# Kernel optimization log

Measured on AMD Instinct MI355X. Metric: run time of the kernel, lower is better.

Reference implementation:

```python
import jax, jax.numpy as jnp
import numpy as np

N = 1_048_576   # sampled points
E = 32          # grid feature dim (static_grid.out_dim / xyzt_grid.out_dim)
H = 64          # hidden_dim
GEO = 15        # geo_feat_dim
V = 3           # input_ch_views


def setup_inputs() -> dict:
    key = jax.random.key(0)
    ks = jax.random.split(key, 32)
    rn = lambda k, s: jax.random.normal(k, s, jnp.float32)
    w = lambda k, i, o: rn(k, (i, o)) * (1.0 / np.sqrt(i))
    inp = {
        'embedded_xyz': rn(ks[0], (N, E)),
        'embedded_xyzt': rn(ks[1], (N, E)),
        'embedded_xyzt_cam': rn(ks[2], (N, E)),
        'input_views': rn(ks[3], (N, V)),
        'keep_mask_bg': (jax.random.uniform(ks[4], (N,)) < 0.95).astype(jnp.float32),
        'keep_mask_fg': (jax.random.uniform(ks[5], (N,)) < 0.95).astype(jnp.float32),
        'keep_mask_actor': (jax.random.uniform(ks[6], (N,)) < 0.95).astype(jnp.float32),
    }
    # sigma nets: E->H, H->H, H->(1+1+GEO); color nets: in->H, H->H, H->H, H->3
    sigma_shapes = [(E, H), (H, H), (H, 1 + 1 + GEO)]
    bg_color_shapes = [(V + GEO, H), (H, H), (H, H), (H, 3)]      # BG uses viewdirs
    dyn_color_shapes = [(GEO, H), (H, H), (H, H), (H, 3)]          # use_viewdirs_FG=False
    ki = 7
    for pref, cshapes in (('bg', bg_color_shapes), ('fg', dyn_color_shapes), ('actor', dyn_color_shapes)):
        for l, (i, o) in enumerate(sigma_shapes):
            inp[f'{pref}_s{l}'] = w(ks[ki], i, o); ki += 1
        for l, (i, o) in enumerate(cshapes):
            inp[f'{pref}_c{l}'] = w(ks[ki], i, o); ki += 1
    return inp


def _mlp(h, Ws):
    # bias-free Linear + ReLU chain, no ReLU after last layer
    for W in Ws[:-1]:
        h = jax.nn.relu(h @ W)
    return h @ Ws[-1]


def _branch(emb, views, sW, cW, mask):
    h = _mlp(emb, sW)                       # [N, 1+1+GEO]
    sigma = jax.nn.softplus(h[:, 0]) * mask # relu_act = Softplus
    geo = h[:, 2:]
    ci = geo if views is None else jnp.concatenate([views, geo], axis=-1)
    color = jax.nn.sigmoid(_mlp(ci, cW)) * mask[:, None]
    return sigma, color


def reference(embedded_xyz, embedded_xyzt, embedded_xyzt_cam, input_views,
              keep_mask_bg, keep_mask_fg, keep_mask_actor,
              bg_s0, bg_s1, bg_s2, bg_c0, bg_c1, bg_c2, bg_c3,
              fg_s0, fg_s1, fg_s2, fg_c0, fg_c1, fg_c2, fg_c3,
              actor_s0, actor_s1, actor_s2, actor_c0, actor_c1, actor_c2, actor_c3):
    bg_sigma, bg_color = _branch(embedded_xyz, input_views,
                                 [bg_s0, bg_s1, bg_s2], [bg_c0, bg_c1, bg_c2, bg_c3], keep_mask_bg)
    fg_sigma, fg_color = _branch(embedded_xyzt, None,
                                 [fg_s0, fg_s1, fg_s2], [fg_c0, fg_c1, fg_c2, fg_c3], keep_mask_fg)
    ac_sigma, ac_color = _branch(embedded_xyzt_cam, None,
                                 [actor_s0, actor_s1, actor_s2], [actor_c0, actor_c1, actor_c2, actor_c3], keep_mask_actor)
    sigma = bg_sigma + fg_sigma + ac_sigma + 1e-9
    color = ((bg_sigma / sigma)[:, None] * bg_color
             + (fg_sigma / sigma)[:, None] * fg_color
             + (ac_sigma / sigma)[:, None] * ac_color)
    return jnp.concatenate([color, sigma[:, None]], axis=-1)  # [N, 4]
```

## Files before the change

### kernel.cpp

```cpp
#include <hip/hip_runtime.h>

typedef unsigned int  uint;
typedef unsigned short ushort;

#define N_PTS  1048576
#define BLOCK  1024
#define WAVES  16
#define NPT    2
#define CHUNK  (WAVES * NPT * 16)
#define NCHUNK (N_PTS / CHUNK)
#define GRID   256

static_assert(N_PTS % CHUNK == 0, "chunking");
static_assert(NCHUNK % GRID == 0, "grid stride");

typedef __attribute__((ext_vector_type(8))) _Float16 f16x8;
typedef __attribute__((ext_vector_type(2))) _Float16 f16x2;
typedef __attribute__((ext_vector_type(4))) float    f32x4;

struct Params {
    const float* emb[3];
    const float* views;
    const float* mask[3];
    const float* w[21];
    float* out;
};

__device__ uint g_wbuf[3 * 9216];

#define OFF_S0 0
#define OFF_S1 2048
#define OFF_S2 6144
#define OFF_C0 7168
#define OFF_C1 9216
#define OFF_C2 13312
#define OFF_C3 17408
#define BR_SZ  18432

__device__ __forceinline__ uint cvt2w(float a, float b) {
    f16x2 v = {(_Float16)a, (_Float16)b};
    return __builtin_bit_cast(uint, v);
}
__device__ __forceinline__ uint cvt2(float a, float b) {
    return __builtin_bit_cast(uint, __builtin_amdgcn_cvt_pkrtz(a, b));
}
__device__ __forceinline__ uint maxz(uint x) {
    f16x2 v = __builtin_bit_cast(f16x2, x);
    f16x2 z = {(_Float16)0.f, (_Float16)0.f};
    return __builtin_bit_cast(uint, __builtin_elementwise_max(v, z));
}

__device__ __forceinline__ f32x4 MFMA(f16x8 a, f16x8 b, f32x4 c) {
    return __builtin_amdgcn_mfma_f32_16x16x32_f16(a, b, c, 0, 0, 0);
}

__device__ __forceinline__ float fast_rcp(float x) { return __builtin_amdgcn_rcpf(x); }

__device__ __forceinline__ float wphys(int L, int br, const float* W, int kp, int m) {
    if (L == 0) return W[kp * 64 + m];
    const int g = (kp & 31) >> 3, e = kp & 7, h = kp >> 5;
    if (L == 3) {
        if (e < 4) {
            const int f = 4 * g + e;
            if (f < 1) return 0.f;
            return (br == 0) ? W[(f + 2) * 64 + m] : W[(f - 1) * 64 + m];
        }
        return (br == 0 && g == 0 && e <= 6) ? W[(e - 4) * 64 + m] : 0.f;
    }
    const int f = 16 * ((e >> 2) + 2 * h) + 4 * g + (e & 3);
    if (L == 2) return W[f * 17 + (m == 0 ? 0 : m + 1)];
    if (L == 6) return (m < 3) ? W[f * 3 + m] : 0.f;
    return W[f * 64 + m];
}

__global__ void prep_weights(Params P) {
    const int idx = blockIdx.x * 256 + threadIdx.x;
    const int br  = idx / 9216;
    const int rem = idx - br * 9216;
    int L, q;
    if      (rem < 1024) { L = 0; q = rem;        }
    else if (rem < 3072) { L = 1; q = rem - 1024; }
    else if (rem < 3584) { L = 2; q = rem - 3072; }
    else if (rem < 4608) { L = 3; q = rem - 3584; }
    else if (rem < 6656) { L = 4; q = rem - 4608; }
    else if (rem < 8704) { L = 5; q = rem - 6656; }
    else                 { L = 6; q = rem - 8704; }
    const float* W   = P.w[br * 7 + L];
    const int kk_n   = (L == 0 || L == 3) ? 1 : 2;
    const int E  = q * 2;
    const int b  = E >> 9;
    const int ln = (E >> 3) & 63;
    const int e  = E & 7;
    const int mt = b / kk_n;
    const int kk = b - mt * kk_n;
    const int m  = mt * 16 + (ln & 15);
    const int kp = kk * 32 + (ln >> 4) * 8 + e;
    g_wbuf[idx] = cvt2w(wphys(L, br, W, kp, m), wphys(L, br, W, kp + 1, m));
}

template<bool RELU>
__device__ __forceinline__ void handoff64(const f32x4 (&a)[4], uint4 &b0, uint4 &b1) {
#pragma unroll
    for (int h = 0; h < 2; ++h) {
        const f32x4 &lo = a[2 * h], &hi = a[2 * h + 1];
        uint w0 = cvt2(lo[0], lo[1]);
        uint w1 = cvt2(lo[2], lo[3]);
        uint w2 = cvt2(hi[0], hi[1]);
        uint w3 = cvt2(hi[2], hi[3]);
        if (RELU) { w0 = maxz(w0); w1 = maxz(w1); w2 = maxz(w2); w3 = maxz(w3); }
        uint4 &b = h ? b1 : b0;
        b.x = w0; b.y = w1; b.z = w2; b.w = w3;
    }
}

__device__ __forceinline__ void layer64(const ushort* lw, int lane,
                                        const uint4 (&b0)[NPT], const uint4 (&b1)[NPT],
                                        f32x4 (&acc)[NPT][4]) {
    f16x8 wf[8];
#pragma unroll
    for (int b = 0; b < 8; ++b) wf[b] = *(const f16x8*)(lw + b * 512 + lane * 8);
#pragma unroll
    for (int t = 0; t < NPT; ++t) {
        const f16x8 i0 = __builtin_bit_cast(f16x8, b0[t]);
        const f16x8 i1 = __builtin_bit_cast(f16x8, b1[t]);
#pragma unroll
        for (int mt = 0; mt < 4; ++mt) {
            f32x4 a = (f32x4){0.f, 0.f, 0.f, 0.f};
            a = MFMA(wf[mt * 2 + 0], i0, a);
            a = MFMA(wf[mt * 2 + 1], i1, a);
            acc[t][mt] = a;
        }
    }
}

__global__ __launch_bounds__(BLOCK, 4) void nerf_main(Params P) {
    __shared__ __align__(16) ushort lds_w[3 * BR_SZ];

    const int tid = threadIdx.x;
    {
        const uint4* src = (const uint4*)g_wbuf;
        uint4* dst = (uint4*)lds_w;
        for (int i = tid; i < 6912; i += BLOCK) dst[i] = src[i];
    }
    __syncthreads();

    const int wave = tid >> 6;
    const int lane = tid & 63;
    const int c = lane & 15;
    const int g = lane >> 4;

#pragma unroll 1
    for (int ch = blockIdx.x; ch < NCHUNK; ch += gridDim.x) {
        const int p0 = ch * CHUNK + wave * (NPT * 16);

        float stot[NPT], car[NPT], cag[NPT], cab[NPT];
#pragma unroll
        for (int t = 0; t < NPT; ++t) { stot[t] = 0.f; car[t] = 0.f; cag[t] = 0.f; cab[t] = 0.f; }

#pragma unroll 1
        for (int br = 0; br < 3; ++br) {
            const ushort* lw  = lds_w + br * BR_SZ;
            const float* emb  = P.emb[br];
            const float* msk  = P.mask[br];
            float sig_pre[NPT], rp[NPT], gp[NPT], bp[NPT];
            uint4 b0[NPT], b1[NPT];
            f32x4 acc[NPT][4];

            {
                f16x8 wf[4];
#pragma unroll
                for (int b = 0; b < 4; ++b)
                    wf[b] = *(const f16x8*)(lw + OFF_S0 + b * 512 + lane * 8);
#pragma unroll
                for (int t = 0; t < NPT; ++t) {
                    const float* ep = emb + (size_t)(p0 + t * 16 + c) * 32 + g * 8;
                    const float4 ea = *(const float4*)ep;
                    const float4 eb = *(const float4*)(ep + 4);
                    uint4 iv;
                    iv.x = cvt2(ea.x, ea.y); iv.y = cvt2(ea.z, ea.w);
                    iv.z = cvt2(eb.x, eb.y); iv.w = cvt2(eb.z, eb.w);
                    const f16x8 inf = __builtin_bit_cast(f16x8, iv);
#pragma unroll
                    for (int mt = 0; mt < 4; ++mt) {
                        f32x4 a = (f32x4){0.f, 0.f, 0.f, 0.f};
                        acc[t][mt] = MFMA(wf[mt], inf, a);
                    }
                }
            }
#pragma unroll
            for (int t = 0; t < NPT; ++t) handoff64<true>(acc[t], b0[t], b1[t]);

            layer64(lw + OFF_S1, lane, b0, b1, acc);
#pragma unroll
            for (int t = 0; t < NPT; ++t) handoff64<true>(acc[t], b0[t], b1[t]);

            {
                const f16x8 w0 = *(const f16x8*)(lw + OFF_S2 + 0 * 512 + lane * 8);
                const f16x8 w1 = *(const f16x8*)(lw + OFF_S2 + 1 * 512 + lane * 8);
#pragma unroll
                for (int t = 0; t < NPT; ++t) {
                    f32x4 a = (f32x4){0.f, 0.f, 0.f, 0.f};
                    a = MFMA(w0, __builtin_bit_cast(f16x8, b0[t]), a);
                    a = MFMA(w1, __builtin_bit_cast(f16x8, b1[t]), a);
                    sig_pre[t] = a[0];
                    uint4 nb;
                    nb.x = cvt2(a[0], a[1]);
                    nb.y = cvt2(a[2], a[3]);
                    nb.z = 0u; nb.w = 0u;
                    if (br == 0 && g == 0) {
                        const float* vp = P.views + (size_t)(p0 + t * 16 + c) * 3;
                        nb.z = cvt2(vp[0], vp[1]);
                        nb.w = cvt2(vp[2], 0.f);
                    }
                    b0[t] = nb;
                }
            }

            {
                f16x8 wf[4];
#pragma unroll
                for (int b = 0; b < 4; ++b)
                    wf[b] = *(const f16x8*)(lw + OFF_C0 + b * 512 + lane * 8);
#pragma unroll
                for (int t = 0; t < NPT; ++t) {
                    const f16x8 inf = __builtin_bit_cast(f16x8, b0[t]);
#pragma unroll
                    for (int mt = 0; mt < 4; ++mt) {
                        f32x4 a = (f32x4){0.f, 0.f, 0.f, 0.f};
                        acc[t][mt] = MFMA(wf[mt], inf, a);
                    }
                }
            }
#pragma unroll
            for (int t = 0; t < NPT; ++t) handoff64<true>(acc[t], b0[t], b1[t]);

            layer64(lw + OFF_C1, lane, b0, b1, acc);
#pragma unroll
            for (int t = 0; t < NPT; ++t) handoff64<true>(acc[t], b0[t], b1[t]);
            layer64(lw + OFF_C2, lane, b0, b1, acc);
#pragma unroll
            for (int t = 0; t < NPT; ++t) handoff64<true>(acc[t], b0[t], b1[t]);

            {
                const f16x8 w0 = *(const f16x8*)(lw + OFF_C3 + 0 * 512 + lane * 8);
                const f16x8 w1 = *(const f16x8*)(lw + OFF_C3 + 1 * 512 + lane * 8);
#pragma unroll
                for (int t = 0; t < NPT; ++t) {
                    f32x4 a = (f32x4){0.f, 0.f, 0.f, 0.f};
                    a = MFMA(w0, __builtin_bit_cast(f16x8, b0[t]), a);
                    a = MFMA(w1, __builtin_bit_cast(f16x8, b1[t]), a);
                    rp[t] = a[0]; gp[t] = a[1]; bp[t] = a[2];
                }
            }

#pragma unroll
            for (int t = 0; t < NPT; ++t) {
                const float mk = msk[p0 + t * 16 + c];
                const float x  = sig_pre[t];
                const float ex = __expf(x);
                const float sp = (x > 15.f) ? x : 0.69314718f * __log2f(1.f + ex);
                const float sb = sp * mk;
                stot[t] += sb;
                const float sm = sb * mk;
                car[t] += sm * fast_rcp(1.f + __expf(-rp[t]));
                cag[t] += sm * fast_rcp(1.f + __expf(-gp[t]));
                cab[t] += sm * fast_rcp(1.f + __expf(-bp[t]));
            }
        }

#pragma unroll
        for (int t = 0; t < NPT; ++t) {
            if (lane < 16) {
                const float s   = stot[t] + 1e-9f;
                const float inv = fast_rcp(s);
                float4 o;
                o.x = car[t] * inv; o.y = cag[t] * inv; o.z = cab[t] * inv; o.w = s;
                *(float4*)(P.out + (size_t)(p0 + t * 16 + lane) * 4) = o;
            }
        }
    }
}

extern "C" void kernel_launch(void* const* d_in, const int* in_sizes, int n_in,
                              void* d_out, int out_size, void* d_ws, size_t ws_size,
                              hipStream_t stream) {
    (void)in_sizes; (void)n_in; (void)d_ws; (void)ws_size; (void)out_size;
    Params P;
    P.emb[0] = (const float*)d_in[0];
    P.emb[1] = (const float*)d_in[1];
    P.emb[2] = (const float*)d_in[2];
    P.views  = (const float*)d_in[3];
    P.mask[0] = (const float*)d_in[4];
    P.mask[1] = (const float*)d_in[5];
    P.mask[2] = (const float*)d_in[6];
    for (int i = 0; i < 21; ++i) P.w[i] = (const float*)d_in[7 + i];
    P.out = (float*)d_out;
    prep_weights<<<108, 256, 0, stream>>>(P);
    nerf_main<<<GRID, BLOCK, 0, stream>>>(P);
}
```

Measured before the change: 130.4 us.

## Process four point-tiles per wave and convert accumulators per tile inline

```diff
diff --git a/kernel.cpp b/kernel.cpp
--- a/kernel.cpp
+++ b/kernel.cpp
@@ -6,7 +6,7 @@
 #define N_PTS  1048576
 #define BLOCK  1024
 #define WAVES  16
-#define NPT    2
+#define NPT    4
 #define CHUNK  (WAVES * NPT * 16)
 #define NCHUNK (N_PTS / CHUNK)
 #define GRID   256
@@ -114,8 +114,7 @@
 }
 
 __device__ __forceinline__ void layer64(const ushort* lw, int lane,
-                                        const uint4 (&b0)[NPT], const uint4 (&b1)[NPT],
-                                        f32x4 (&acc)[NPT][4]) {
+                                        uint4 (&b0)[NPT], uint4 (&b1)[NPT]) {
     f16x8 wf[8];
 #pragma unroll
     for (int b = 0; b < 8; ++b) wf[b] = *(const f16x8*)(lw + b * 512 + lane * 8);
@@ -123,13 +122,15 @@
     for (int t = 0; t < NPT; ++t) {
         const f16x8 i0 = __builtin_bit_cast(f16x8, b0[t]);
         const f16x8 i1 = __builtin_bit_cast(f16x8, b1[t]);
+        f32x4 acc[4];
 #pragma unroll
         for (int mt = 0; mt < 4; ++mt) {
             f32x4 a = (f32x4){0.f, 0.f, 0.f, 0.f};
             a = MFMA(wf[mt * 2 + 0], i0, a);
             a = MFMA(wf[mt * 2 + 1], i1, a);
-            acc[t][mt] = a;
-        }
+            acc[mt] = a;
+        }
+        handoff64<true>(acc, b0[t], b1[t]);
     }
 }
 
@@ -164,7 +165,6 @@
             const float* msk  = P.mask[br];
             float sig_pre[NPT], rp[NPT], gp[NPT], bp[NPT];
             uint4 b0[NPT], b1[NPT];
-            f32x4 acc[NPT][4];
 
             {
                 f16x8 wf[4];
@@ -180,19 +180,17 @@
                     iv.x = cvt2(ea.x, ea.y); iv.y = cvt2(ea.z, ea.w);
                     iv.z = cvt2(eb.x, eb.y); iv.w = cvt2(eb.z, eb.w);
                     const f16x8 inf = __builtin_bit_cast(f16x8, iv);
+                    f32x4 acc[4];
 #pragma unroll
                     for (int mt = 0; mt < 4; ++mt) {
                         f32x4 a = (f32x4){0.f, 0.f, 0.f, 0.f};
-                        acc[t][mt] = MFMA(wf[mt], inf, a);
+                        acc[mt] = MFMA(wf[mt], inf, a);
                     }
-                }
-            }
-#pragma unroll
-            for (int t = 0; t < NPT; ++t) handoff64<true>(acc[t], b0[t], b1[t]);
-
-            layer64(lw + OFF_S1, lane, b0, b1, acc);
-#pragma unroll
-            for (int t = 0; t < NPT; ++t) handoff64<true>(acc[t], b0[t], b1[t]);
+                    handoff64<true>(acc, b0[t], b1[t]);
+                }
+            }
+
+            layer64(lw + OFF_S1, lane, b0, b1);
 
             {
                 const f16x8 w0 = *(const f16x8*)(lw + OFF_S2 + 0 * 512 + lane * 8);
@@ -224,22 +222,18 @@
 #pragma unroll
                 for (int t = 0; t < NPT; ++t) {
                     const f16x8 inf = __builtin_bit_cast(f16x8, b0[t]);
+                    f32x4 acc[4];
 #pragma unroll
                     for (int mt = 0; mt < 4; ++mt) {
                         f32x4 a = (f32x4){0.f, 0.f, 0.f, 0.f};
-                        acc[t][mt] = MFMA(wf[mt], inf, a);
+                        acc[mt] = MFMA(wf[mt], inf, a);
                     }
-                }
-            }
-#pragma unroll
-            for (int t = 0; t < NPT; ++t) handoff64<true>(acc[t], b0[t], b1[t]);
-
-            layer64(lw + OFF_C1, lane, b0, b1, acc);
-#pragma unroll
-            for (int t = 0; t < NPT; ++t) handoff64<true>(acc[t], b0[t], b1[t]);
-            layer64(lw + OFF_C2, lane, b0, b1, acc);
-#pragma unroll
-            for (int t = 0; t < NPT; ++t) handoff64<true>(acc[t], b0[t], b1[t]);
+                    handoff64<true>(acc, b0[t], b1[t]);
+                }
+            }
+
+            layer64(lw + OFF_C1, lane, b0, b1);
+            layer64(lw + OFF_C2, lane, b0, b1);
 
             {
                 const f16x8 w0 = *(const f16x8*)(lw + OFF_C3 + 0 * 512 + lane * 8);
```

New measurement: 138.6 us. 6.3% more time.
